# Performance work log

Measured on AMD Instinct MI355X. Metric: run time of the kernel, lower is better.

The kernel has to match this reference:

```python
import jax, jax.numpy as jnp
import numpy as np

NUM_HEADS = 16
TEMPERATURE = 1.0


def setup_inputs() -> dict:
    key = jax.random.key(0)
    ks = jax.random.split(key, 6)
    B, H = 2048, 2048
    return {
        "hidden_states": jax.random.normal(ks[0], (B, H), dtype=jnp.float32),
        "attention_mask": jnp.ones((B,), dtype=bool),
        "Wq": jax.random.normal(ks[1], (H, H), dtype=jnp.float32) * 0.02,
        "Wk": jax.random.normal(ks[2], (H, H), dtype=jnp.float32) * 0.02,
        "Wv": jax.random.normal(ks[3], (H, H), dtype=jnp.float32) * 0.02,
        "Wo": jax.random.normal(ks[4], (H, H), dtype=jnp.float32) * 0.02,
        "scale_param": jnp.full((1,), -3.0, dtype=jnp.float32),
    }


def reference(hidden_states, attention_mask, Wq, Wk, Wv, Wo, scale_param):
    B, H = hidden_states.shape
    nh = NUM_HEADS
    hd = H // nh
    # projections (torch Linear: x @ W.T), reshape to [heads, batch, head_dim]
    q = (hidden_states @ Wq.T).reshape(B, nh, hd).transpose(1, 0, 2)
    k = (hidden_states @ Wk.T).reshape(B, nh, hd).transpose(1, 0, 2)
    v = (hidden_states @ Wv.T).reshape(B, nh, hd).transpose(1, 0, 2)
    # cross-batch scores [heads, B, B]
    scores = jnp.einsum('hqd,hkd->hqk', q, k) / (hd ** 0.5 * TEMPERATURE)
    neg_inf = jnp.float32(-jnp.inf)
    eye = jnp.eye(B, dtype=bool)  # exclude self-attention (diagonal)
    scores = jnp.where(eye[None, :, :], neg_inf, scores)
    scores = jnp.where(attention_mask[None, None, :], scores, neg_inf)
    attn = jax.nn.softmax(scores, axis=-1)
    attn = jnp.nan_to_num(attn, nan=0.0)  # rows fully masked -> 0 (dropout=0 is identity)
    ctx = jnp.einsum('hqk,hkd->hqd', attn, v)  # [heads, B, head_dim]
    ctx = ctx.transpose(1, 0, 2).reshape(B, H)
    cross = ctx @ Wo.T
    scale = jax.nn.sigmoid(scale_param[0])
    return hidden_states + scale * cross
```

## Files before the change

kernel.cpp:

```cpp
#include <hip/hip_runtime.h>

typedef __bf16 bf16;
typedef __attribute__((ext_vector_type(8))) __bf16 bf16x8;
typedef __attribute__((ext_vector_type(4))) float f32x4;
typedef __attribute__((ext_vector_type(4))) short s16x4;

#define HDIM 2048

__device__ __forceinline__ void glds16(const void* g, void* l) {
  __builtin_amdgcn_global_load_lds((const __attribute__((address_space(1))) void*)g,
                                   (__attribute__((address_space(3))) void*)l,
                                   16, 0, 0);
}

#define MFMA16(a, b, c) __builtin_amdgcn_mfma_f32_16x16x32_bf16(a, b, c, 0, 0, 0)

__global__ __launch_bounds__(256) void cvt5(
    const float* __restrict__ s0, const float* __restrict__ s1,
    const float* __restrict__ s2, const float* __restrict__ s3,
    const float* __restrict__ s4,
    bf16* __restrict__ d0, bf16* __restrict__ d1, bf16* __restrict__ d2,
    bf16* __restrict__ d3, bf16* __restrict__ d4) {
  const float* s; bf16* d;
  switch (blockIdx.y) {
    case 0: s = s0; d = d0; break;
    case 1: s = s1; d = d1; break;
    case 2: s = s2; d = d2; break;
    case 3: s = s3; d = d3; break;
    default: s = s4; d = d4; break;
  }
  const size_t base = (size_t)blockIdx.x * 4096 + (threadIdx.x << 2);
  for (int i = 0; i < 4; i++) {
    const float4 v = *(const float4*)(s + base + i * 1024);
    union { bf16 h[4]; s16x4 s4v; } u;
    u.h[0] = (bf16)v.x; u.h[1] = (bf16)v.y; u.h[2] = (bf16)v.z; u.h[3] = (bf16)v.w;
    *(s16x4*)(d + base + i * 1024) = u.s4v;
  }
}

__device__ __forceinline__ void gemm128_core(const bf16* __restrict__ A,
                                             const bf16* __restrict__ B,
                                             int rowBase, int colBase,
                                             f32x4 acc[4][4],
                                             bf16* ldsA, bf16* ldsB) {
  const int t = threadIdx.x;
  const int w = t >> 6, l = t & 63;
  const int wr = (w >> 1) << 6, wc = (w & 1) << 6;
  const int lr = l & 15, lq = l >> 4;

  for (int mi = 0; mi < 4; mi++)
    for (int ni = 0; ni < 4; ni++)
      for (int r = 0; r < 4; r++) acc[mi][ni][r] = 0.f;

  const int sRow = (w << 4) + (l >> 2);
  const int sCol = (l & 3) << 3;
  const bf16* gA = A + (size_t)(rowBase + sRow) * HDIM + sCol;
  const bf16* gB = B + (size_t)(colBase + sRow) * HDIM + sCol;
  bf16* lA = ldsA + (w << 9);
  bf16* lB = ldsB + (w << 9);

  for (int k0 = 0; k0 < HDIM; k0 += 32) {
    glds16(gA, lA);
    glds16(gA + (size_t)64 * HDIM, lA + 2048);
    glds16(gB, lB);
    glds16(gB + (size_t)64 * HDIM, lB + 2048);
    gA += 32; gB += 32;
    __syncthreads();

    bf16x8 af[4], bfr[4];
    for (int mi = 0; mi < 4; mi++)
      af[mi] = *(const bf16x8*)&ldsA[(wr + mi * 16 + lr) * 32 + lq * 8];
    for (int ni = 0; ni < 4; ni++)
      bfr[ni] = *(const bf16x8*)&ldsB[(wc + ni * 16 + lr) * 32 + lq * 8];
    for (int mi = 0; mi < 4; mi++)
      for (int ni = 0; ni < 4; ni++)
        acc[mi][ni] = MFMA16(af[mi], bfr[ni], acc[mi][ni]);
    __syncthreads();
  }
}

__global__ __launch_bounds__(256) void qkv_gemm(
    const bf16* __restrict__ hs, const bf16* __restrict__ Wq,
    const bf16* __restrict__ Wk, const bf16* __restrict__ Wv,
    bf16* __restrict__ qb, bf16* __restrict__ Kf, bf16* __restrict__ Vf) {
  __shared__ bf16 ldsA[128 * 32];
  __shared__ bf16 ldsB[128 * 32];
  const int z = blockIdx.z;
  const bf16* W = (z == 0) ? Wq : (z == 1) ? Wk : Wv;
  const int rowBase = blockIdx.y << 7, colBase = blockIdx.x << 7;
  f32x4 acc[4][4];
  gemm128_core(hs, W, rowBase, colBase, acc, ldsA, ldsB);

  const int t = threadIdx.x;
  const int w = t >> 6, l = t & 63;
  const int wr = (w >> 1) << 6, wc = (w & 1) << 6;
  const int lr = l & 15, lq = l >> 4;

  if (z == 0) {
    for (int mi = 0; mi < 4; mi++)
      for (int ni = 0; ni < 4; ni++) {
        const int col = colBase + wc + ni * 16 + lr;
        const int row0 = rowBase + wr + mi * 16 + lq * 4;
        for (int r = 0; r < 4; r++)
          qb[(size_t)(row0 + r) * HDIM + col] = (bf16)acc[mi][ni][r];
      }
  } else if (z == 1) {
    for (int mi = 0; mi < 4; mi++)
      for (int ni = 0; ni < 4; ni++) {
        const int dim = colBase + wc + ni * 16 + lr;
        const int hh = dim >> 7, ks = (dim >> 5) & 3, kh = (dim >> 3) & 3, j = dim & 7;
        const int row0 = rowBase + wr + mi * 16 + lq * 4;
        for (int r = 0; r < 4; r++) {
          const int key = row0 + r;
          const int kbk = key >> 7, kni = (key >> 4) & 7, kl = key & 15;
          Kf[(((size_t)hh * 16 + kbk) * 32 + kni * 4 + ks) * 512 +
             (kh * 16 + kl) * 8 + j] = (bf16)acc[mi][ni][r];
        }
      }
  } else {
    for (int mi = 0; mi < 4; mi++)
      for (int ni = 0; ni < 4; ni++) {
        const int dim = colBase + wc + ni * 16 + lr;
        const int hh = dim >> 7, vni = (dim >> 4) & 7, ll = dim & 15;
        const int row0 = rowBase + wr + mi * 16 + lq * 4;
        const int kbk = row0 >> 7, ks = (row0 >> 5) & 3, lh = (row0 >> 3) & 3;
        const int j0 = row0 & 7;
        union { bf16 h4[4]; s16x4 v; } u;
        for (int r = 0; r < 4; r++) u.h4[r] = (bf16)acc[mi][ni][r];
        *(s16x4*)&Vf[(((size_t)hh * 16 + kbk) * 32 + vni * 4 + ks) * 512 +
                     (lh * 16 + ll) * 8 + j0] = u.v;
      }
  }
}

__global__ __launch_bounds__(256, 1) void attn_kernel(
    const bf16* __restrict__ qb, const bf16* __restrict__ Kf,
    const bf16* __restrict__ Vf, const unsigned char* __restrict__ amask,
    float* __restrict__ Of, float* __restrict__ lsumBuf) {
  __shared__ bf16 Kl[32 * 512];
  __shared__ bf16 Vl[32 * 512];
  __shared__ bf16 Pl[4 * 32 * 64];

  const int qt = blockIdx.x, h = blockIdx.y, kk = blockIdx.z;
  const int t = threadIdx.x, w = t >> 6, l = t & 63;
  const int lr = l & 15, lq = l >> 4;
  bf16* Pw = Pl + (w << 11);

  bf16x8 aq[2][4];
  for (int mi = 0; mi < 2; mi++)
    for (int ks = 0; ks < 4; ks++)
      aq[mi][ks] = *(const bf16x8*)&qb[(size_t)(qt * 128 + w * 32 + mi * 16 + lr) * HDIM +
                                       h * 128 + ks * 32 + lq * 8];

  f32x4 o[2][8];
  for (int mi = 0; mi < 2; mi++)
    for (int ni = 0; ni < 8; ni++)
      for (int r = 0; r < 4; r++) o[mi][ni][r] = 0.f;
  float lsum[2][4];
  for (int mi = 0; mi < 2; mi++)
    for (int r = 0; r < 4; r++) lsum[mi][r] = 0.f;

  const float c = 0.08838834764831845f * 1.4426950408889634f;

  const size_t headOff = (size_t)h * 16 * 32 * 512;
  const size_t t0Off = headOff + (size_t)(kk * 8) * 32 * 512;
  bf16x8 vtmp[8];
  for (int i = 0; i < 8; i++) {
    const int frag = i * 4 + w;
    glds16(Kf + t0Off + frag * 512 + l * 8, Kl + frag * 512);
  }
  for (int i = 0; i < 8; i++) {
    const int frag = i * 4 + w;
    vtmp[i] = *(const bf16x8*)&Vf[t0Off + frag * 512 + l * 8];
  }

  for (int tt = 0; tt < 8; tt++) {
    const int kbk = kk * 8 + tt;
    __syncthreads();

    for (int i = 0; i < 8; i++) {
      const int frag = i * 4 + w;
      *(bf16x8*)&Vl[frag * 512 + l * 8] = vtmp[i];
    }

    f32x4 s[2][8];
    for (int mi = 0; mi < 2; mi++)
      for (int ni = 0; ni < 8; ni++)
        for (int r = 0; r < 4; r++) s[mi][ni][r] = 0.f;
    for (int ks = 0; ks < 4; ks++) {
      bf16x8 bk[8];
      for (int ni = 0; ni < 8; ni++)
        bk[ni] = *(const bf16x8*)&Kl[(ni * 4 + ks) * 512 + l * 8];
      for (int ni = 0; ni < 8; ni++) {
        s[0][ni] = MFMA16(aq[0][ks], bk[ni], s[0][ni]);
        s[1][ni] = MFMA16(aq[1][ks], bk[ni], s[1][ni]);
      }
    }

    __syncthreads();

    if (tt < 7) {
      const size_t tileOffN = headOff + (size_t)(kbk + 1) * 32 * 512;
      for (int i = 0; i < 8; i++) {
        const int frag = i * 4 + w;
        glds16(Kf + tileOffN + frag * 512 + l * 8, Kl + frag * 512);
      }
      for (int i = 0; i < 8; i++) {
        const int frag = i * 4 + w;
        vtmp[i] = *(const bf16x8*)&Vf[tileOffN + frag * 512 + l * 8];
      }
    }

    float am[8];
    for (int ni = 0; ni < 8; ni++)
      am[ni] = amask[kbk * 128 + ni * 16 + lr] ? 0.f : -1e30f;
    if (kbk == qt) {
      for (int mi = 0; mi < 2; mi++)
        for (int ni = 0; ni < 8; ni++) {
          const int colL = ni * 16 + lr;
          for (int r = 0; r < 4; r++) {
            const int rowL = w * 32 + mi * 16 + lq * 4 + r;
            float p = __builtin_exp2f(s[mi][ni][r] * c + am[ni]);
            if (colL == rowL) p = 0.f;
            s[mi][ni][r] = p;
            lsum[mi][r] += p;
          }
        }
    } else {
      for (int mi = 0; mi < 2; mi++)
        for (int ni = 0; ni < 8; ni++)
          for (int r = 0; r < 4; r++) {
            const float p = __builtin_exp2f(s[mi][ni][r] * c + am[ni]);
            s[mi][ni][r] = p;
            lsum[mi][r] += p;
          }
    }

    for (int p = 0; p < 2; p++) {
      for (int mi = 0; mi < 2; mi++)
        for (int nip = 0; nip < 4; nip++) {
          const int ni = p * 4 + nip;
          for (int r = 0; r < 4; r++) {
            const int rl = lq * 4 + r;
            Pw[(mi * 16 + rl) * 64 + (((nip * 2 + (lr >> 3)) ^ (rl & 7)) << 3) +
               (lr & 7)] = (bf16)s[mi][ni][r];
          }
        }
      for (int ksp = 0; ksp < 2; ksp++) {
        const int ks = p * 2 + ksp;
        bf16x8 bv[8];
        for (int ni = 0; ni < 8; ni++)
          bv[ni] = *(const bf16x8*)&Vl[(ni * 4 + ks) * 512 + l * 8];
        const int rchunk = ((ksp * 4 + lq) ^ (lr & 7)) << 3;
        const bf16x8 ap0 = *(const bf16x8*)&Pw[lr * 64 + rchunk];
        const bf16x8 ap1 = *(const bf16x8*)&Pw[(16 + lr) * 64 + rchunk];
        for (int ni = 0; ni < 8; ni++) {
          o[0][ni] = MFMA16(ap0, bv[ni], o[0][ni]);
          o[1][ni] = MFMA16(ap1, bv[ni], o[1][ni]);
        }
      }
    }
  }

  for (int mi = 0; mi < 2; mi++)
    for (int r = 0; r < 4; r++)
      for (int off = 1; off < 16; off <<= 1)
        lsum[mi][r] += __shfl_xor(lsum[mi][r], off);

  const size_t obase = (size_t)kk * ((size_t)HDIM * HDIM);
  for (int mi = 0; mi < 2; mi++)
    for (int ni = 0; ni < 8; ni++)
      for (int r = 0; r < 4; r++) {
        const int row = qt * 128 + w * 32 + mi * 16 + lq * 4 + r;
        const int col = h * 128 + ni * 16 + lr;
        Of[obase + (size_t)row * HDIM + col] = o[mi][ni][r];
      }
  if (lr == 0)
    for (int mi = 0; mi < 2; mi++)
      for (int r = 0; r < 4; r++) {
        const int row = qt * 128 + w * 32 + mi * 16 + lq * 4 + r;
        lsumBuf[((size_t)kk * 16 + h) * 2048 + row] = lsum[mi][r];
      }
}

__global__ __launch_bounds__(256) void combine_kernel(
    const float* __restrict__ Of, const float* __restrict__ lsumBuf,
    bf16* __restrict__ ctx) {
  const size_t base = (size_t)blockIdx.x * 2048 + ((size_t)threadIdx.x << 3);
  const int row = (int)(base >> 11);
  const int h = ((int)base & 2047) >> 7;
  const float lt = lsumBuf[h * 2048 + row] + lsumBuf[(16 + h) * 2048 + row];
  const float linv = (lt > 0.f) ? 1.f / lt : 0.f;
  const float* p0 = Of + base;
  const float* p1 = Of + (size_t)4194304 + base;
  const float4 a0 = *(const float4*)p0;
  const float4 a1 = *(const float4*)(p0 + 4);
  const float4 b0 = *(const float4*)p1;
  const float4 b1 = *(const float4*)(p1 + 4);
  union { bf16 hh[8]; s16x4 v[2]; } u;
  u.hh[0] = (bf16)((a0.x + b0.x) * linv);
  u.hh[1] = (bf16)((a0.y + b0.y) * linv);
  u.hh[2] = (bf16)((a0.z + b0.z) * linv);
  u.hh[3] = (bf16)((a0.w + b0.w) * linv);
  u.hh[4] = (bf16)((a1.x + b1.x) * linv);
  u.hh[5] = (bf16)((a1.y + b1.y) * linv);
  u.hh[6] = (bf16)((a1.z + b1.z) * linv);
  u.hh[7] = (bf16)((a1.w + b1.w) * linv);
  *(s16x4*)(ctx + base) = u.v[0];
  *(s16x4*)(ctx + base + 4) = u.v[1];
}

__global__ __launch_bounds__(256) void out_gemm(
    const bf16* __restrict__ ctx, const bf16* __restrict__ Wo,
    const float* __restrict__ hs, const float* __restrict__ scale_p,
    float* __restrict__ outp) {
  __shared__ bf16 ldsA[128 * 32];
  __shared__ bf16 ldsB[64 * 32];
  const int rowBase = blockIdx.y << 7, colBase = blockIdx.x << 6;
  const int t = threadIdx.x;
  const int w = t >> 6, l = t & 63;
  const int wr = (w >> 1) << 6, wc = (w & 1) << 5;
  const int lr = l & 15, lq = l >> 4;

  f32x4 acc[4][2];
  for (int mi = 0; mi < 4; mi++)
    for (int ni = 0; ni < 2; ni++)
      for (int r = 0; r < 4; r++) acc[mi][ni][r] = 0.f;

  const int sRow = (w << 4) + (l >> 2);
  const int sCol = (l & 3) << 3;
  const bf16* gA = ctx + (size_t)(rowBase + sRow) * HDIM + sCol;
  const bf16* gB = Wo + (size_t)(colBase + sRow) * HDIM + sCol;
  bf16* lA = ldsA + (w << 9);
  bf16* lB = ldsB + (w << 9);

  for (int k0 = 0; k0 < HDIM; k0 += 32) {
    glds16(gA, lA);
    glds16(gA + (size_t)64 * HDIM, lA + 2048);
    glds16(gB, lB);
    gA += 32; gB += 32;
    __syncthreads();

    bf16x8 af[4], bfr[2];
    for (int mi = 0; mi < 4; mi++)
      af[mi] = *(const bf16x8*)&ldsA[(wr + mi * 16 + lr) * 32 + lq * 8];
    for (int ni = 0; ni < 2; ni++)
      bfr[ni] = *(const bf16x8*)&ldsB[(wc + ni * 16 + lr) * 32 + lq * 8];
    for (int mi = 0; mi < 4; mi++)
      for (int ni = 0; ni < 2; ni++)
        acc[mi][ni] = MFMA16(af[mi], bfr[ni], acc[mi][ni]);
    __syncthreads();
  }

  const float sig = 1.0f / (1.0f + __expf(-scale_p[0]));
  for (int mi = 0; mi < 4; mi++)
    for (int ni = 0; ni < 2; ni++) {
      const int col = colBase + wc + ni * 16 + lr;
      const int row0 = rowBase + wr + mi * 16 + lq * 4;
      for (int r = 0; r < 4; r++) {
        const size_t idx = (size_t)(row0 + r) * HDIM + col;
        outp[idx] = hs[idx] + sig * acc[mi][ni][r];
      }
    }
}

extern "C" void kernel_launch(void* const* d_in, const int* in_sizes, int n_in,
                              void* d_out, int out_size, void* d_ws, size_t ws_size,
                              hipStream_t stream) {
  const float* hs = (const float*)d_in[0];
  const unsigned char* amask = (const unsigned char*)d_in[1];
  const float* Wq = (const float*)d_in[2];
  const float* Wk = (const float*)d_in[3];
  const float* Wv = (const float*)d_in[4];
  const float* Wo = (const float*)d_in[5];
  const float* scale_p = (const float*)d_in[6];
  float* outp = (float*)d_out;

  const size_t N = (size_t)HDIM * HDIM;
  bf16* qb   = (bf16*)d_ws;
  bf16* Kf   = qb + N;
  bf16* Vf   = Kf + N;
  bf16* ctx  = Vf + N;
  bf16* hs16 = ctx + N;
  bf16* Wq16 = hs16 + N;
  bf16* Wk16 = Wq16 + N;
  bf16* Wv16 = Wk16 + N;
  bf16* Wo16 = Wv16 + N;
  float* Of = (float*)hs16;
  float* lsumBuf = (float*)d_out;

  cvt5<<<dim3(1024, 5), 256, 0, stream>>>(hs, Wq, Wk, Wv, Wo,
                                          hs16, Wq16, Wk16, Wv16, Wo16);
  qkv_gemm<<<dim3(16, 16, 3), 256, 0, stream>>>(hs16, Wq16, Wk16, Wv16, qb, Kf, Vf);
  attn_kernel<<<dim3(16, 16, 2), 256, 0, stream>>>(qb, Kf, Vf, amask, Of, lsumBuf);
  combine_kernel<<<dim3(2048), 256, 0, stream>>>(Of, lsumBuf, ctx);
  out_gemm<<<dim3(32, 16), 256, 0, stream>>>(ctx, Wo16, hs, scale_p, outp);
}
```

Baseline: 309.0 us.

## Double-buffer K/V tiles in attention, 512-thread blocks sharing K/V across 256 queries

The attention kernel now runs 8 waves per block covering 256 query rows, so each K/V tile loaded into LDS is reused by twice as many queries. K and V are double-buffered in LDS via direct global-to-LDS loads, which removes the register staging of V and cuts the syncs per tile to one. The score tile is processed in two 64-column halves to reduce register pressure. LDS use roughly doubles and the grid halves to 256 blocks, which lowers parallelism on a chip with many CUs.

Measured after the change: 275.8 us (median of 2 runs). -10.7%, faster.

```diff
diff --git a/kernel.cpp b/kernel.cpp
--- a/kernel.cpp
+++ b/kernel.cpp
@@ -133,13 +133,13 @@
   }
 }
 
-__global__ __launch_bounds__(256, 1) void attn_kernel(
+__global__ __launch_bounds__(512, 2) void attn_kernel(
     const bf16* __restrict__ qb, const bf16* __restrict__ Kf,
     const bf16* __restrict__ Vf, const unsigned char* __restrict__ amask,
     float* __restrict__ Of, float* __restrict__ lsumBuf) {
-  __shared__ bf16 Kl[32 * 512];
-  __shared__ bf16 Vl[32 * 512];
-  __shared__ bf16 Pl[4 * 32 * 64];
+  __shared__ bf16 Kl[2][32 * 512];
+  __shared__ bf16 Vl[2][32 * 512];
+  __shared__ bf16 Pl[8 * 32 * 64];
 
   const int qt = blockIdx.x, h = blockIdx.y, kk = blockIdx.z;
   const int t = threadIdx.x, w = t >> 6, l = t & 63;
@@ -149,7 +149,7 @@
   bf16x8 aq[2][4];
   for (int mi = 0; mi < 2; mi++)
     for (int ks = 0; ks < 4; ks++)
-      aq[mi][ks] = *(const bf16x8*)&qb[(size_t)(qt * 128 + w * 32 + mi * 16 + lr) * HDIM +
+      aq[mi][ks] = *(const bf16x8*)&qb[(size_t)(qt * 256 + w * 32 + mi * 16 + lr) * HDIM +
                                        h * 128 + ks * 32 + lq * 8];
 
   f32x4 o[2][8];
@@ -163,94 +163,90 @@
   const float c = 0.08838834764831845f * 1.4426950408889634f;
 
   const size_t headOff = (size_t)h * 16 * 32 * 512;
-  const size_t t0Off = headOff + (size_t)(kk * 8) * 32 * 512;
-  bf16x8 vtmp[8];
-  for (int i = 0; i < 8; i++) {
-    const int frag = i * 4 + w;
-    glds16(Kf + t0Off + frag * 512 + l * 8, Kl + frag * 512);
-  }
-  for (int i = 0; i < 8; i++) {
-    const int frag = i * 4 + w;
-    vtmp[i] = *(const bf16x8*)&Vf[t0Off + frag * 512 + l * 8];
+  const int diagTile = qt * 2 + (w >> 2);
+
+  {
+    const size_t t0 = headOff + (size_t)(kk * 8) * 32 * 512;
+    for (int i = 0; i < 4; i++) {
+      const int frag = i * 8 + w;
+      glds16(Kf + t0 + frag * 512 + l * 8, &Kl[0][frag * 512]);
+    }
+    for (int i = 0; i < 4; i++) {
+      const int frag = i * 8 + w;
+      glds16(Vf + t0 + frag * 512 + l * 8, &Vl[0][frag * 512]);
+    }
   }
 
   for (int tt = 0; tt < 8; tt++) {
     const int kbk = kk * 8 + tt;
-    __syncthreads();
-
-    for (int i = 0; i < 8; i++) {
-      const int frag = i * 4 + w;
-      *(bf16x8*)&Vl[frag * 512 + l * 8] = vtmp[i];
-    }
-
-    f32x4 s[2][8];
-    for (int mi = 0; mi < 2; mi++)
-      for (int ni = 0; ni < 8; ni++)
-        for (int r = 0; r < 4; r++) s[mi][ni][r] = 0.f;
-    for (int ks = 0; ks < 4; ks++) {
-      bf16x8 bk[8];
-      for (int ni = 0; ni < 8; ni++)
-        bk[ni] = *(const bf16x8*)&Kl[(ni * 4 + ks) * 512 + l * 8];
-      for (int ni = 0; ni < 8; ni++) {
-        s[0][ni] = MFMA16(aq[0][ks], bk[ni], s[0][ni]);
-        s[1][ni] = MFMA16(aq[1][ks], bk[ni], s[1][ni]);
-      }
-    }
+    const int buf = tt & 1;
 
     __syncthreads();
 
     if (tt < 7) {
-      const size_t tileOffN = headOff + (size_t)(kbk + 1) * 32 * 512;
-      for (int i = 0; i < 8; i++) {
-        const int frag = i * 4 + w;
-        glds16(Kf + tileOffN + frag * 512 + l * 8, Kl + frag * 512);
-      }
-      for (int i = 0; i < 8; i++) {
-        const int frag = i * 4 + w;
-        vtmp[i] = *(const bf16x8*)&Vf[tileOffN + frag * 512 + l * 8];
-      }
-    }
-
-    float am[8];
-    for (int ni = 0; ni < 8; ni++)
-      am[ni] = amask[kbk * 128 + ni * 16 + lr] ? 0.f : -1e30f;
-    if (kbk == qt) {
+      const size_t tN = headOff + (size_t)(kbk + 1) * 32 * 512;
+      for (int i = 0; i < 4; i++) {
+        const int frag = i * 8 + w;
+        glds16(Kf + tN + frag * 512 + l * 8, &Kl[buf ^ 1][frag * 512]);
+      }
+      for (int i = 0; i < 4; i++) {
+        const int frag = i * 8 + w;
+        glds16(Vf + tN + frag * 512 + l * 8, &Vl[buf ^ 1][frag * 512]);
+      }
+    }
+
+    for (int half = 0; half < 2; half++) {
+      f32x4 s[2][4];
       for (int mi = 0; mi < 2; mi++)
-        for (int ni = 0; ni < 8; ni++) {
-          const int colL = ni * 16 + lr;
-          for (int r = 0; r < 4; r++) {
-            const int rowL = w * 32 + mi * 16 + lq * 4 + r;
-            float p = __builtin_exp2f(s[mi][ni][r] * c + am[ni]);
-            if (colL == rowL) p = 0.f;
-            s[mi][ni][r] = p;
-            lsum[mi][r] += p;
+        for (int ni = 0; ni < 4; ni++)
+          for (int r = 0; r < 4; r++) s[mi][ni][r] = 0.f;
+      for (int ks = 0; ks < 4; ks++) {
+        bf16x8 bk[4];
+        for (int ni = 0; ni < 4; ni++)
+          bk[ni] = *(const bf16x8*)&Kl[buf][((half * 4 + ni) * 4 + ks) * 512 + l * 8];
+        for (int ni = 0; ni < 4; ni++) {
+          s[0][ni] = MFMA16(aq[0][ks], bk[ni], s[0][ni]);
+          s[1][ni] = MFMA16(aq[1][ks], bk[ni], s[1][ni]);
+        }
+      }
+
+      float am[4];
+      for (int ni = 0; ni < 4; ni++)
+        am[ni] = amask[kbk * 128 + half * 64 + ni * 16 + lr] ? 0.f : -1e30f;
+      if (kbk == diagTile) {
+        for (int mi = 0; mi < 2; mi++)
+          for (int ni = 0; ni < 4; ni++) {
+            const int colL = half * 64 + ni * 16 + lr;
+            for (int r = 0; r < 4; r++) {
+              const int rowL = (w & 3) * 32 + mi * 16 + lq * 4 + r;
+              float p = __builtin_exp2f(s[mi][ni][r] * c + am[ni]);
+              if (colL == rowL) p = 0.f;
+              s[mi][ni][r] = p;
+              lsum[mi][r] += p;
+            }
           }
-        }
-    } else {
+      } else {
+        for (int mi = 0; mi < 2; mi++)
+          for (int ni = 0; ni < 4; ni++)
+            for (int r = 0; r < 4; r++) {
+              const float p = __builtin_exp2f(s[mi][ni][r] * c + am[ni]);
+              s[mi][ni][r] = p;
+              lsum[mi][r] += p;
+            }
+      }
+
       for (int mi = 0; mi < 2; mi++)
-        for (int ni = 0; ni < 8; ni++)
-          for (int r = 0; r < 4; r++) {
-            const float p = __builtin_exp2f(s[mi][ni][r] * c + am[ni]);
-            s[mi][ni][r] = p;
-            lsum[mi][r] += p;
-          }
-    }
-
-    for (int p = 0; p < 2; p++) {
-      for (int mi = 0; mi < 2; mi++)
-        for (int nip = 0; nip < 4; nip++) {
-          const int ni = p * 4 + nip;
+        for (int ni = 0; ni < 4; ni++)
           for (int r = 0; r < 4; r++) {
             const int rl = lq * 4 + r;
-            Pw[(mi * 16 + rl) * 64 + (((nip * 2 + (lr >> 3)) ^ (rl & 7)) << 3) +
+            Pw[(mi * 16 + rl) * 64 + (((ni * 2 + (lr >> 3)) ^ (rl & 7)) << 3) +
                (lr & 7)] = (bf16)s[mi][ni][r];
           }
-        }
+
       for (int ksp = 0; ksp < 2; ksp++) {
-        const int ks = p * 2 + ksp;
         bf16x8 bv[8];
         for (int ni = 0; ni < 8; ni++)
-          bv[ni] = *(const bf16x8*)&Vl[(ni * 4 + ks) * 512 + l * 8];
+          bv[ni] = *(const bf16x8*)&Vl[buf][(ni * 4 + half * 2 + ksp) * 512 + l * 8];
         const int rchunk = ((ksp * 4 + lq) ^ (lr & 7)) << 3;
         const bf16x8 ap0 = *(const bf16x8*)&Pw[lr * 64 + rchunk];
         const bf16x8 ap1 = *(const bf16x8*)&Pw[(16 + lr) * 64 + rchunk];
@@ -271,14 +267,14 @@
   for (int mi = 0; mi < 2; mi++)
     for (int ni = 0; ni < 8; ni++)
       for (int r = 0; r < 4; r++) {
-        const int row = qt * 128 + w * 32 + mi * 16 + lq * 4 + r;
+        const int row = qt * 256 + w * 32 + mi * 16 + lq * 4 + r;
         const int col = h * 128 + ni * 16 + lr;
         Of[obase + (size_t)row * HDIM + col] = o[mi][ni][r];
       }
   if (lr == 0)
     for (int mi = 0; mi < 2; mi++)
       for (int r = 0; r < 4; r++) {
-        const int row = qt * 128 + w * 32 + mi * 16 + lq * 4 + r;
+        const int row = qt * 256 + w * 32 + mi * 16 + lq * 4 + r;
         lsumBuf[((size_t)kk * 16 + h) * 2048 + row] = lsum[mi][r];
       }
 }
@@ -392,7 +388,7 @@
   cvt5<<<dim3(1024, 5), 256, 0, stream>>>(hs, Wq, Wk, Wv, Wo,
                                           hs16, Wq16, Wk16, Wv16, Wo16);
   qkv_gemm<<<dim3(16, 16, 3), 256, 0, stream>>>(hs16, Wq16, Wk16, Wv16, qb, Kf, Vf);
-  attn_kernel<<<dim3(16, 16, 2), 256, 0, stream>>>(qb, Kf, Vf, amask, Of, lsumBuf);
+  attn_kernel<<<dim3(8, 16, 2), 512, 0, stream>>>(qb, Kf, Vf, amask, Of, lsumBuf);
   combine_kernel<<<dim3(2048), 256, 0, stream>>>(Of, lsumBuf, ctx);
   out_gemm<<<dim3(32, 16), 256, 0, stream>>>(ctx, Wo16, hs, scale_p, outp);
 }
```
